# Optimization experiments

Hardware: AMD Instinct MI355X
Metric: run time of the kernel (lower is better)

The kernel has to match this reference:

```python
import math
import jax, jax.numpy as jnp
import numpy as np

D_MODEL = 1024
N_HEADS = 16
HEAD_DIM = 64          # block_size
NUM_RULES = 64
RANK = 8               # proj_rank = round(sqrt(head_dim)); also router_rank
SHARED_RANK = 32       # round(sqrt(d_model))
NUM_BLOCKS = 16        # min(in,out)//block_size = 1024//64; total_block_dim == d_model
B, S = 4, 1024
ROPE_BASE = 10000.0


def setup_inputs() -> dict:
    key = jax.random.key(0)
    ks = iter(jax.random.split(key, 32))
    def nrm(shape, s=0.02):
        return jax.random.normal(next(ks), shape, dtype=jnp.float32) * s
    inp = {
        "x": jax.random.normal(next(ks), (B, S, D_MODEL), dtype=jnp.float32),
        "target_rule_ids": jax.random.randint(next(ks), (B, S), 0, NUM_RULES),
    }
    for p in ("q", "k", "v", "o"):
        inp[p + "_si"] = nrm((D_MODEL, SHARED_RANK))
        inp[p + "_so"] = nrm((SHARED_RANK, D_MODEL))
        inp[p + "_ri"] = nrm((NUM_RULES, HEAD_DIM, RANK))
        inp[p + "_ro"] = nrm((NUM_RULES, RANK, HEAD_DIM))
        inp[p + "_lg"] = nrm((NUM_RULES, NUM_BLOCKS), 1.0 / math.sqrt(NUM_BLOCKS))
    inp["router_q"] = nrm((NUM_RULES, RANK))
    inp["router_k"] = nrm((NUM_RULES, RANK))
    return inp


def _rule_proj(x, rules, si, so, ri, ro, lg):
    """RuleAwareProjection.forward_rules_batched, de-permuted.

    The torch code argsorts tokens by rule, zero-pads per-rule buckets, runs
    bmm per rule and scatters back; mathematically that equals a per-token
    gather of the rule's low-rank adapter, which is what we compute here.
    x: [N, D_MODEL], rules: [N] int.
    """
    base = (x @ si) @ so                                  # shared low-rank path
    xb = x.reshape(-1, NUM_BLOCKS, HEAD_DIM)              # [N, nb, bs]
    h = jnp.einsum('nbs,nsr->nbr', xb, ri[rules])         # [N, nb, rank]
    a = jnp.einsum('nbr,nrt->nbt', h, ro[rules])          # [N, nb, bs]
    # temperature = 1/sqrt(num_blocks) => logits / temperature = logits*sqrt(nb)
    sel = jax.nn.softmax(lg[rules] * math.sqrt(NUM_BLOCKS), axis=-1)
    return base + (a * sel[:, :, None]).reshape(-1, D_MODEL)


def _rope(q, k):
    # q, k: [B, H, S, D]; interleaved-pair rotation, start_pos = 0.
    S_, D = q.shape[2], q.shape[3]
    pos = jnp.arange(S_, dtype=jnp.float32)[:, None]
    div = jnp.exp(jnp.arange(0, D, 2, dtype=jnp.float32) * (-math.log(ROPE_BASE) / D))
    f = pos * div                                         # [S, D/2]
    sin, cos = jnp.sin(f), jnp.cos(f)
    def rot(t):
        t1, t2 = t[..., 0::2], t[..., 1::2]
        return jnp.stack([t1 * cos - t2 * sin, t2 * cos + t1 * sin], axis=-1).reshape(t.shape)
    return rot(q), rot(k)


def reference(x, target_rule_ids,
              q_si, q_so, q_ri, q_ro, q_lg,
              k_si, k_so, k_ri, k_ro, k_lg,
              v_si, v_so, v_ri, v_ro, v_lg,
              o_si, o_so, o_ri, o_ro, o_lg,
              router_q, router_k):
    B_, S_, C = x.shape
    flat_x = x.reshape(-1, C)
    rules = target_rule_ids.reshape(-1)

    q = _rule_proj(flat_x, rules, q_si, q_so, q_ri, q_ro, q_lg)
    k = _rule_proj(flat_x, rules, k_si, k_so, k_ri, k_ro, k_lg)
    v = _rule_proj(flat_x, rules, v_si, v_so, v_ri, v_ro, v_lg)
    q = q.reshape(B_, S_, N_HEADS, HEAD_DIM).transpose(0, 2, 1, 3)
    k = k.reshape(B_, S_, N_HEADS, HEAD_DIM).transpose(0, 2, 1, 3)
    v = v.reshape(B_, S_, N_HEADS, HEAD_DIM).transpose(0, 2, 1, 3)
    q, k = _rope(q, k)

    # rule-routing sparse mask: cosine affinity between token rule embeddings
    rq = router_q[target_rule_ids]                        # [B, S, rank]
    rk = router_k[target_rule_ids]
    rqn = rq / jnp.maximum(jnp.linalg.norm(rq, axis=-1, keepdims=True), 1e-12)
    rkn = rk / jnp.maximum(jnp.linalg.norm(rk, axis=-1, keepdims=True), 1e-12)
    tau = 1.0 / math.log(max(math.e, RANK))
    aff = jnp.einsum('bqr,bkr->bqk', rqn, rkn) / tau       # [B, S, S]
    causal = jnp.tril(jnp.ones((S_, S_), dtype=bool))
    masked = jnp.where(causal[None], aff, -jnp.inf)
    top_k = max(2, int(math.sqrt(S_)))
    if S_ > top_k:
        thr = jax.lax.top_k(masked, top_k)[0][..., -1:]
        rule_mask = (masked >= thr) & causal[None]
    else:
        rule_mask = jnp.broadcast_to(causal[None], masked.shape)

    scores = jnp.einsum('bhqd,bhkd->bhqk', q, k) / math.sqrt(HEAD_DIM)
    scores = jnp.where(rule_mask[:, None], scores, -jnp.inf)
    attn = jax.nn.softmax(scores, axis=-1)
    out = jnp.einsum('bhqk,bhkd->bhqd', attn, v)
    out = out.transpose(0, 2, 1, 3).reshape(-1, C)
    out = _rule_proj(out, rules, o_si, o_so, o_ri, o_ro, o_lg)
    return out.reshape(B_, S_, C)
```

## Files before the change

kernel.cpp:

```cpp
#include <hip/hip_runtime.h>
#include <hip/hip_bf16.h>

#define D_MODEL 1024
#define N_HEADS 16
#define HEAD_DIM 64
#define NUM_RULES 64
#define RANK 8
#define SHARED_RANK 32
#define NUM_BLOCKS_ 16
#define BB 4
#define SS 1024
#define NTOK (BB*SS)
#define NGRP (NTOK/8)
#define NGRP4 (NTOK/4)

typedef __attribute__((ext_vector_type(8))) short bf16x8;
typedef __attribute__((ext_vector_type(4))) float f32x4;

__device__ __forceinline__ float bf2f(unsigned short u) {
  unsigned int i = ((unsigned int)u) << 16;
  float f;
  __builtin_memcpy(&f, &i, 4);
  return f;
}
__device__ __forceinline__ unsigned short f2bf(float f) {
  __hip_bfloat16 h = __float2bfloat16(f);
  unsigned short u;
  __builtin_memcpy(&u, &h, 2);
  return u;
}
__device__ __forceinline__ float u2f(unsigned int i) {
  float f;
  __builtin_memcpy(&f, &i, 4);
  return f;
}
template<bool BF>
__device__ __forceinline__ float ldw(const void* p, size_t i) {
  if (BF) return bf2f(((const unsigned short*)p)[i]);
  else    return ((const float*)p)[i];
}

__global__ void detect_kernel(const unsigned short* __restrict__ x, int* __restrict__ flag) {
  const int lane = threadIdx.x;
  int good = 0;
  for (int i = 0; i < 4; i++) {
    unsigned short u = x[lane*4 + i];
    int e = (u >> 7) & 0xFF;
    good += (e == 0 || (e >= 100 && e <= 145)) ? 1 : 0;
  }
  for (int off = 32; off; off >>= 1) good += __shfl_xor(good, off);
  if (lane == 0) flag[0] = (good >= 224) ? 1 : 0;
}

template<bool BF>
__device__ __forceinline__ void precompute_body(
    const void* rq, const void* rk,
    const void* qlg, const void* klg, const void* vlg, const void* olg,
    float* __restrict__ M, float* __restrict__ sel)
{
  __shared__ float rqn[64][8], rkn[64][8];
  const int tid = threadIdx.x;
  if (tid < 64) {
    float v[8]; float s = 0.f;
    for (int i = 0; i < 8; i++) { v[i] = ldw<BF>(rq, tid*8+i); s += v[i]*v[i]; }
    float inv = 1.0f / fmaxf(sqrtf(s), 1e-12f);
    for (int i = 0; i < 8; i++) rqn[tid][i] = v[i]*inv;
  } else if (tid < 128) {
    int r = tid - 64;
    float v[8]; float s = 0.f;
    for (int i = 0; i < 8; i++) { v[i] = ldw<BF>(rk, r*8+i); s += v[i]*v[i]; }
    float inv = 1.0f / fmaxf(sqrtf(s), 1e-12f);
    for (int i = 0; i < 8; i++) rkn[r][i] = v[i]*inv;
  }
  __syncthreads();
  const float LN8 = 2.0794415416798357f;
  for (int idx = tid; idx < 64*64; idx += 256) {
    int i = idx >> 6, j = idx & 63;
    float d = 0.f;
    for (int t = 0; t < 8; t++) d += rqn[i][t]*rkn[j][t];
    M[idx] = d * LN8;
  }
  const void* lgs[4] = {qlg, klg, vlg, olg};
  {
    int r = tid & 63;
    const void* lg = lgs[tid >> 6];
    float e[NUM_BLOCKS_]; float mx = -1e30f;
    for (int b = 0; b < NUM_BLOCKS_; b++) {
      e[b] = ldw<BF>(lg, r*NUM_BLOCKS_ + b) * 4.0f;
      mx = fmaxf(mx, e[b]);
    }
    float s = 0.f;
    for (int b = 0; b < NUM_BLOCKS_; b++) { e[b] = expf(e[b]-mx); s += e[b]; }
    float inv = 1.0f/s;
    for (int b = 0; b < NUM_BLOCKS_; b++) sel[tid*NUM_BLOCKS_+b] = e[b]*inv;
  }
}

__global__ void precompute_kernel(
    const void* rq, const void* rk,
    const void* qlg, const void* klg, const void* vlg, const void* olg,
    float* M, float* sel, const int* __restrict__ flag)
{
  if (*flag) precompute_body<true >(rq, rk, qlg, klg, vlg, olg, M, sel);
  else       precompute_body<false>(rq, rk, qlg, klg, vlg, olg, M, sel);
}

__global__ __launch_bounds__(128) void prep_wb_kernel(
    const float* __restrict__ qsi, const float* __restrict__ ksi,
    const float* __restrict__ vsi, const float* __restrict__ osi,
    unsigned short* __restrict__ wh, unsigned short* __restrict__ wl,
    const int* __restrict__ flag)
{
  if (*flag) return;
  const int kt = blockIdx.x, p = blockIdx.y;
  const int tid = threadIdx.x, nt = tid >> 6, lane = tid & 63;
  const float* si = (p==0)?qsi:((p==1)?ksi:((p==2)?vsi:osi));
  const int col = nt*16 + (lane & 15);
  const int k0 = kt*32 + (lane >> 4)*8;
  size_t base = ((((size_t)p*32 + kt)*2 + nt)*64 + lane)*8;
  unsigned short h8[8], l8[8];
  #pragma unroll
  for (int j = 0; j < 8; j++) {
    float f = si[(size_t)(k0 + j)*SHARED_RANK + col];
    unsigned short hu = f2bf(f);
    h8[j] = hu;
    l8[j] = f2bf(f - bf2f(hu));
  }
  #pragma unroll
  for (int j = 0; j < 8; j++) { wh[base + j] = h8[j]; wl[base + j] = l8[j]; }
}

template<int NPROJ>
__device__ __forceinline__ void tt_mfma_body(
    const float* __restrict__ xin,
    const unsigned short* __restrict__ wh, const unsigned short* __restrict__ wl,
    int p0, float* __restrict__ ttg)
{
  const int NT = NPROJ*2;
  const int tile = blockIdx.x;
  const int tid = threadIdx.x, lane = tid & 63, w = tid >> 6;
  const int kq = lane >> 4;
  __shared__ float red[4][64][25];

  f32x4 acc[NT];
  #pragma unroll
  for (int i = 0; i < NT; i++) acc[i] = (f32x4){0.f,0.f,0.f,0.f};

  const float* xrow = xin + (size_t)(tile*16 + (lane & 15))*D_MODEL + kq*8;
  #pragma unroll 2
  for (int s = 0; s < 8; s++) {
    const int kt = w*8 + s;
    float4 a0 = *(const float4*)(xrow + kt*32);
    float4 a1 = *(const float4*)(xrow + kt*32 + 4);
    float av[8] = {a0.x,a0.y,a0.z,a0.w,a1.x,a1.y,a1.z,a1.w};
    bf16x8 ah, al;
    #pragma unroll
    for (int j = 0; j < 8; j++) {
      unsigned short hu = f2bf(av[j]);
      ah[j] = (short)hu;
      al[j] = (short)f2bf(av[j] - bf2f(hu));
    }
    #pragma unroll
    for (int p = 0; p < NPROJ; p++) {
      #pragma unroll
      for (int nt = 0; nt < 2; nt++) {
        size_t bidx = ((((size_t)(p0+p)*32 + kt)*2 + nt)*64 + lane)*8;
        bf16x8 bh = *(const bf16x8*)(wh + bidx);
        bf16x8 bl = *(const bf16x8*)(wl + bidx);
        f32x4 c = acc[p*2+nt];
        c = __builtin_amdgcn_mfma_f32_16x16x32_bf16(ah, bh, c, 0, 0, 0);
        c = __builtin_amdgcn_mfma_f32_16x16x32_bf16(al, bh, c, 0, 0, 0);
        c = __builtin_amdgcn_mfma_f32_16x16x32_bf16(ah, bl, c, 0, 0, 0);
        acc[p*2+nt] = c;
      }
    }
  }
  #pragma unroll
  for (int i = 0; i < NT; i++) {
    red[w][lane][i*4+0] = acc[i][0]; red[w][lane][i*4+1] = acc[i][1];
    red[w][lane][i*4+2] = acc[i][2]; red[w][lane][i*4+3] = acc[i][3];
  }
  __syncthreads();
  if (w == 0) {
    const int tok0 = tile*16 + (lane >> 4)*4;
    #pragma unroll
    for (int i = 0; i < NT; i++) {
      const int ys = i >> 1, jj = (i & 1)*16 + (lane & 15);
      #pragma unroll
      for (int r = 0; r < 4; r++) {
        float sum = red[0][lane][i*4+r] + red[1][lane][i*4+r]
                  + red[2][lane][i*4+r] + red[3][lane][i*4+r];
        ttg[((size_t)ys*NTOK + tok0 + r)*32 + jj] = sum;
      }
    }
  }
}

__global__ __launch_bounds__(256) void A_tt_mfma3(
    const float* __restrict__ xin,
    const unsigned short* __restrict__ wh, const unsigned short* __restrict__ wl,
    float* __restrict__ ttg, const int* __restrict__ flag)
{
  if (*flag) return;
  tt_mfma_body<3>(xin, wh, wl, 0, ttg);
}

__global__ __launch_bounds__(256) void A_tt_mfma1(
    const float* __restrict__ xin,
    const unsigned short* __restrict__ wh, const unsigned short* __restrict__ wl,
    float* __restrict__ ttg, const int* __restrict__ flag)
{
  if (*flag) return;
  tt_mfma_body<1>(xin, wh, wl, 3, ttg);
}

template<int NP>
__device__ __forceinline__ void hh_body(
    const float* __restrict__ xin, const int* __restrict__ rules,
    const float* __restrict__ ri0, const float* __restrict__ ri1,
    const float* __restrict__ ri2, float* __restrict__ hhg)
{
  const int g = blockIdx.x, n0 = g*8, tid = threadIdx.x;
  const int t = tid >> 5, blk = (tid >> 1) & 15, r0 = (tid & 1)*4;
  const int n = n0 + t;
  const int rule = rules[n];
  const float* xb = xin + (size_t)n*D_MODEL + blk*64;
  const float* wb[3];
  wb[0] = ri0 + (size_t)rule*512 + r0;
  if (NP > 1) {
    wb[1] = ri1 + (size_t)rule*512 + r0;
    wb[2] = ri2 + (size_t)rule*512 + r0;
  }
  float a[NP][4];
  #pragma unroll
  for (int p = 0; p < NP; p++) { a[p][0]=0.f; a[p][1]=0.f; a[p][2]=0.f; a[p][3]=0.f; }
  #pragma unroll 4
  for (int k4 = 0; k4 < 16; k4++) {
    float4 xv = *(const float4*)(xb + k4*4);
    #pragma unroll
    for (int q = 0; q < 4; q++) {
      const int k = k4*4 + q;
      float xq = (q==0)?xv.x:((q==1)?xv.y:((q==2)?xv.z:xv.w));
      #pragma unroll
      for (int p = 0; p < NP; p++) {
        float4 wv = *(const float4*)(wb[p] + (size_t)k*8);
        a[p][0] += xq*wv.x; a[p][1] += xq*wv.y; a[p][2] += xq*wv.z; a[p][3] += xq*wv.w;
      }
    }
  }
  #pragma unroll
  for (int p = 0; p < NP; p++) {
    float4 hv; hv.x=a[p][0]; hv.y=a[p][1]; hv.z=a[p][2]; hv.w=a[p][3];
    *(float4*)&hhg[((size_t)p*NTOK + n)*128 + blk*8 + r0] = hv;
  }
}

__global__ __launch_bounds__(256) void A_hh3_f32(
    const float* __restrict__ xin, const int* __restrict__ rules,
    const float* __restrict__ qri, const float* __restrict__ kri,
    const float* __restrict__ vri, float* __restrict__ hhg,
    const int* __restrict__ flag)
{
  if (*flag) return;
  hh_body<3>(xin, rules, qri, kri, vri, hhg);
}

__global__ __launch_bounds__(256) void A_hh1_f32(
    const float* __restrict__ xin, const int* __restrict__ rules,
    const float* __restrict__ ori, float* __restrict__ hhg,
    const int* __restrict__ flag)
{
  if (*flag) return;
  hh_body<1>(xin, rules, ori, ori, ori, hhg);
}

template<bool IN_BF, bool W_BF>
__device__ __forceinline__ void stageA_body(
    const void* __restrict__ xin, const int* __restrict__ rules,
    const void* __restrict__ si, const void* __restrict__ ri,
    float* __restrict__ ttg, float* __restrict__ hhg, int yslot)
{
  const int g = blockIdx.x, n0 = g*8, tid = threadIdx.x;
  __shared__ float xs[8][D_MODEL];
  __shared__ float tpart[8][32][9];
  __shared__ int rl[8];

  #pragma unroll
  for (int t = 0; t < 8; t++) {
    float4 f;
    if (IN_BF) {
      ushort4 u = ((const ushort4*)((const unsigned short*)xin + (size_t)(n0+t)*D_MODEL))[tid];
      f.x = bf2f(u.x); f.y = bf2f(u.y); f.z = bf2f(u.z); f.w = bf2f(u.w);
    } else {
      f = ((const float4*)xin)[(size_t)(n0+t)*(D_MODEL/4) + tid];
    }
    *(float4*)&xs[t][tid*4] = f;
  }
  if (tid < 8) rl[tid] = rules[n0 + tid];
  __syncthreads();

  {
    const int c = tid >> 5, j = tid & 31;
    float p[8];
    #pragma unroll
    for (int t = 0; t < 8; t++) p[t] = 0.f;
    #pragma unroll 4
    for (int d4 = 0; d4 < 32; d4++) {
      const int d = c*128 + d4*4;
      float w0 = ldw<W_BF>(si, (size_t)(d+0)*SHARED_RANK + j);
      float w1 = ldw<W_BF>(si, (size_t)(d+1)*SHARED_RANK + j);
      float w2 = ldw<W_BF>(si, (size_t)(d+2)*SHARED_RANK + j);
      float w3 = ldw<W_BF>(si, (size_t)(d+3)*SHARED_RANK + j);
      #pragma unroll
      for (int t = 0; t < 8; t++) {
        float4 xv = *(const float4*)&xs[t][d];
        p[t] += xv.x*w0 + xv.y*w1 + xv.z*w2 + xv.w*w3;
      }
    }
    #pragma unroll
    for (int t = 0; t < 8; t++) tpart[c][j][t] = p[t];
  }
  __syncthreads();

  {
    const int t = tid >> 5, j = tid & 31;
    float s = 0.f;
    #pragma unroll
    for (int c = 0; c < 8; c++) s += tpart[c][j][t];
    ttg[((size_t)yslot*NTOK + n0 + t)*32 + j] = s;
  }
  {
    const int t = tid >> 5, blk = (tid >> 1) & 15, r0 = (tid & 1)*4;
    const int rule = rl[t];
    float a0=0.f, a1=0.f, a2=0.f, a3=0.f;
    #pragma unroll 4
    for (int k4 = 0; k4 < 16; k4++) {
      const int kk = ((k4 + blk) & 15) * 4;
      float4 xv = *(const float4*)&xs[t][blk*64 + kk];
      #pragma unroll
      for (int q = 0; q < 4; q++) {
        const int k = kk + q;
        float w0,w1,w2,w3;
        if (W_BF) {
          ushort4 u = *(const ushort4*)((const unsigned short*)ri + (size_t)rule*512 + (size_t)k*8 + r0);
          w0=bf2f(u.x); w1=bf2f(u.y); w2=bf2f(u.z); w3=bf2f(u.w);
        } else {
          float4 u = *(const float4*)((const float*)ri + (size_t)rule*512 + (size_t)k*8 + r0);
          w0=u.x; w1=u.y; w2=u.z; w3=u.w;
        }
        float xq = (q==0)?xv.x:((q==1)?xv.y:((q==2)?xv.z:xv.w));
        a0 += xq*w0; a1 += xq*w1; a2 += xq*w2; a3 += xq*w3;
      }
    }
    float4 hv; hv.x=a0; hv.y=a1; hv.z=a2; hv.w=a3;
    *(float4*)&hhg[((size_t)yslot*NTOK + n0 + t)*128 + blk*8 + r0] = hv;
  }
}

__global__ __launch_bounds__(256) void A_qkv_bf16(
    const void* x, const int* rules,
    const void* qsi, const void* qri, const void* ksi, const void* kri,
    const void* vsi, const void* vri,
    float* ttg, float* hhg, const int* __restrict__ flag)
{
  if (!*flag) return;
  const int y = blockIdx.y;
  const void* si = (y==0)?qsi:((y==1)?ksi:vsi);
  const void* ri = (y==0)?qri:((y==1)?kri:vri);
  stageA_body<true,true>(x, rules, si, ri, ttg, hhg, y);
}

__global__ __launch_bounds__(256) void A_o_bf16(
    const void* ain, const int* rules, const void* osi, const void* ori,
    float* ttg, float* hhg, const int* __restrict__ flag)
{
  if (!*flag) return;
  stageA_body<false,true>(ain, rules, osi, ori, ttg, hhg, 0);
}

template<bool W_BF>
__device__ __forceinline__ void stageB_body(
    const float* __restrict__ ttg, const float* __restrict__ hhg,
    const int* __restrict__ rules,
    const void* __restrict__ so, const void* __restrict__ ro,
    const float* __restrict__ sel, void* __restrict__ out,
    int yslot, int do_rope, int out_bf)
{
  const int blk4 = blockIdx.x;
  const int n0 = blk4*4, tid = threadIdx.x;
  __shared__ float tt_lds[32][5];
  __shared__ float hh_lds[4][132];
  __shared__ int rl[4];

  if (tid < 128) {
    const int j = tid >> 2, t4 = tid & 3;
    tt_lds[j][t4] = ttg[((size_t)yslot*NTOK + n0 + t4)*32 + j];
  } else if (tid < 256 && (tid - 128) < 128) {
    const int i = tid - 128;
    const int t4 = i >> 5, c = (i*4) & 127;
    float4 hv = *(const float4*)&hhg[((size_t)yslot*NTOK + n0 + t4)*128 + c];
    *(float4*)&hh_lds[t4][c] = hv;
  }
  if (tid < 4) rl[tid] = rules[n0 + tid];
  __syncthreads();

  const int ch0 = tid*4;
  float a0[4], a1[4], a2[4], a3[4];
  #pragma unroll
  for (int t = 0; t < 4; t++) { a0[t]=0.f; a1[t]=0.f; a2[t]=0.f; a3[t]=0.f; }

  #pragma unroll 4
  for (int j = 0; j < 32; j++) {
    float w0, w1, w2, w3;
    if (W_BF) {
      ushort4 u = *(const ushort4*)((const unsigned short*)so + (size_t)j*D_MODEL + ch0);
      w0=bf2f(u.x); w1=bf2f(u.y); w2=bf2f(u.z); w3=bf2f(u.w);
    } else {
      float4 u = *(const float4*)((const float*)so + (size_t)j*D_MODEL + ch0);
      w0=u.x; w1=u.y; w2=u.z; w3=u.w;
    }
    #pragma unroll
    for (int t = 0; t < 4; t++) {
      float tv = tt_lds[j][t];
      a0[t] += tv*w0; a1[t] += tv*w1; a2[t] += tv*w2; a3[t] += tv*w3;
    }
  }

  const int blk = ch0 >> 6, tc = ch0 & 63;
  float inv0 = 0.f, inv1 = 0.f;
  if (do_rope) {
    inv0 = expf(-(float)tc     * (9.210340371976184f/64.0f));
    inv1 = expf(-(float)(tc+2) * (9.210340371976184f/64.0f));
  }
  #pragma unroll 2
  for (int t = 0; t < 4; t++) {
    const int rule = rl[t];
    float b0=0.f, b1=0.f, b2=0.f, b3=0.f;
    #pragma unroll
    for (int r = 0; r < 8; r++) {
      float w0,w1,w2,w3;
      if (W_BF) {
        ushort4 u = *(const ushort4*)((const unsigned short*)ro + (size_t)rule*512 + r*64 + tc);
        w0=bf2f(u.x); w1=bf2f(u.y); w2=bf2f(u.z); w3=bf2f(u.w);
      } else {
        float4 u = *(const float4*)((const float*)ro + (size_t)rule*512 + r*64 + tc);
        w0=u.x; w1=u.y; w2=u.z; w3=u.w;
      }
      float hv = hh_lds[t][blk*8 + r];
      b0 += hv*w0; b1 += hv*w1; b2 += hv*w2; b3 += hv*w3;
    }
    float sb = sel[rule*NUM_BLOCKS_ + blk];
    float e0 = a0[t] + b0*sb, o0 = a1[t] + b1*sb;
    float e1 = a2[t] + b2*sb, o1 = a3[t] + b3*sb;
    const int n = n0 + t;
    if (do_rope) {
      float spos = (float)(n & (SS-1));
      float sn0, cs0, sn1, cs1;
      sincosf(spos*inv0, &sn0, &cs0);
      sincosf(spos*inv1, &sn1, &cs1);
      float u0 = e0*cs0 - o0*sn0; o0 = o0*cs0 + e0*sn0; e0 = u0;
      float u1 = e1*cs1 - o1*sn1; o1 = o1*cs1 + e1*sn1; e1 = u1;
    }
    if (out_bf) {
      ushort4 uv; uv.x=f2bf(e0); uv.y=f2bf(o0); uv.z=f2bf(e1); uv.w=f2bf(o1);
      *(ushort4*)((unsigned short*)out + (size_t)n*D_MODEL + ch0) = uv;
    } else {
      float4 fv; fv.x=e0; fv.y=o0; fv.z=e1; fv.w=o1;
      *(float4*)((float*)out + (size_t)n*D_MODEL + ch0) = fv;
    }
  }
}

__global__ __launch_bounds__(256) void B_qkv(
    const float* ttg, const float* hhg, const int* rules,
    const void* qso, const void* qro, const void* kso, const void* kro,
    const void* vso, const void* vro,
    const float* sel, float* qb, unsigned short* kb, unsigned short* vb,
    const int* __restrict__ flag)
{
  const int y = blockIdx.y;
  const void* so = (y==0)?qso:((y==1)?kso:vso);
  const void* ro = (y==0)?qro:((y==1)?kro:vro);
  void* out = (y==0)?(void*)qb:((y==1)?(void*)kb:(void*)vb);
  if (*flag)
    stageB_body<true >(ttg, hhg, rules, so, ro, sel + y*1024, out, y, (y<2)?1:0, (y>=1)?1:0);
  else
    stageB_body<false>(ttg, hhg, rules, so, ro, sel + y*1024, out, y, (y<2)?1:0, (y>=1)?1:0);
}

__global__ __launch_bounds__(256) void B_o(
    const float* ttg, const float* hhg, const int* rules,
    const void* oso, const void* oro, const float* sel, void* out,
    const int* __restrict__ flag)
{
  if (*flag) stageB_body<true >(ttg, hhg, rules, oso, oro, sel, out, 0, 0, 1);
  else       stageB_body<false>(ttg, hhg, rules, oso, oro, sel, out, 0, 0, 0);
}

__global__ __launch_bounds__(64) void mask_kernel(
    const int* __restrict__ rules, const float* __restrict__ M,
    unsigned long long* __restrict__ am, unsigned int* __restrict__ rp)
{
  const int bid = blockIdx.x;
  const int b = bid >> 10, qi = bid & 1023;
  const int lane = threadIdx.x;
  __shared__ int rrow[SS];
  __shared__ float val[64];
  __shared__ int cnth[64];
  for (int i = lane; i < SS/4; i += 64)
    ((int4*)rrow)[i] = ((const int4*)(rules + b*SS))[i];
  cnth[lane] = 0;
  __syncthreads();
  if (qi < 16 && lane < 16) {
    unsigned v = 0;
    #pragma unroll
    for (int nt = 0; nt < 4; nt++)
      v |= ((unsigned)rrow[qi*64 + nt*16 + lane] & 0xffu) << (8*nt);
    rp[b*256 + qi*16 + lane] = v;
  }
  for (int k = lane; k <= qi; k += 64) atomicAdd(&cnth[rrow[k]], 1);
  const int qrule = rrow[qi];
  const float myv = M[qrule*64 + lane];
  val[lane] = myv;
  __syncthreads();
  const int c = cnth[lane];
  int A = 0;
  for (int r = 0; r < 64; r++) {
    int cr = __shfl(c, r);
    A += (val[r] > myv) ? cr : 0;
  }
  unsigned long long allowed = __ballot(A < 32);
  if (lane == 0) am[bid] = allowed;
}

__global__ __launch_bounds__(256) void vtrans_kernel(
    const unsigned short* __restrict__ vb, unsigned short* __restrict__ vt)
{
  const int st = blockIdx.x, h = blockIdx.y, b = blockIdx.z;
  __shared__ unsigned short t[64][72];
  const int tid = threadIdx.x;
  #pragma unroll
  for (int it = 0; it < 2; it++) {
    int i = tid + it*256;
    int r = i >> 3, c8 = (i & 7)*8;
    uint4 v = *(const uint4*)(vb + ((size_t)(b*SS + st*64 + r)*D_MODEL + h*HEAD_DIM + c8));
    t[c8+0][r] = (unsigned short)(v.x & 0xffffu);
    t[c8+1][r] = (unsigned short)(v.x >> 16);
    t[c8+2][r] = (unsigned short)(v.y & 0xffffu);
    t[c8+3][r] = (unsigned short)(v.y >> 16);
    t[c8+4][r] = (unsigned short)(v.z & 0xffffu);
    t[c8+5][r] = (unsigned short)(v.z >> 16);
    t[c8+6][r] = (unsigned short)(v.w & 0xffffu);
    t[c8+7][r] = (unsigned short)(v.w >> 16);
  }
  __syncthreads();
  #pragma unroll
  for (int it = 0; it < 2; it++) {
    int i = tid + it*256;
    int d = i >> 3, c8 = i & 7;
    uint4 o = *(const uint4*)&t[d][c8*8];
    *(uint4*)(vt + ((size_t)(b*N_HEADS + h)*HEAD_DIM + d)*SS + st*64 + c8*8) = o;
  }
}

__global__ __launch_bounds__(256, 4) void attn_mfma_kernel(
    const float* __restrict__ qb,
    const unsigned short* __restrict__ kb,
    const unsigned short* __restrict__ vtb,
    const unsigned int* __restrict__ rp,
    const unsigned long long* __restrict__ am,
    float* outb)
{
  const int x = blockIdx.x, b = blockIdx.y, h = blockIdx.z;
  const int qt = (x < 8) ? x : (23 - x);
  const int tid = threadIdx.x, lane = tid & 63, w = tid >> 6;
  __shared__ unsigned short Ks[64*64];
  __shared__ unsigned short Vs[64*64];
  __shared__ unsigned short Pl[4][16*64];

  const unsigned short* kbase = kb + (size_t)b*SS*D_MODEL + h*HEAD_DIM;
  const unsigned short* vbase = vtb + (size_t)(b*N_HEADS + h)*HEAD_DIM*SS;
  const unsigned int* rpb = rp + b*256;

  const int srow = tid >> 3;
  const int spos = tid & 7;
  const int kc0 = (srow*8      + (spos ^ (srow        & 7)))*8;
  const int kc1 = ((srow+32)*8 + (spos ^ ((srow+32)   & 7)))*8;
  unsigned short* pw = &Pl[w][0];

  const int qa = qt*64 + w*16 + (lane & 15);
  bf16x8 qfrag[2];
  {
    const float* qrow = qb + (size_t)(b*SS + qa)*D_MODEL + h*HEAD_DIM + (lane>>4)*8;
    #pragma unroll
    for (int kc = 0; kc < 2; kc++) {
      float4 f0 = *(const float4*)(qrow + kc*32);
      float4 f1 = *(const float4*)(qrow + kc*32 + 4);
      bf16x8 qv;
      qv[0] = (short)f2bf(f0.x*0.125f); qv[1] = (short)f2bf(f0.y*0.125f);
      qv[2] = (short)f2bf(f0.z*0.125f); qv[3] = (short)f2bf(f0.w*0.125f);
      qv[4] = (short)f2bf(f1.x*0.125f); qv[5] = (short)f2bf(f1.y*0.125f);
      qv[6] = (short)f2bf(f1.z*0.125f); qv[7] = (short)f2bf(f1.w*0.125f);
      qfrag[kc] = qv;
    }
  }
  int qg[4]; unsigned aqlo[4], aqhi[4];
  #pragma unroll
  for (int r = 0; r < 4; r++) {
    qg[r] = qt*64 + w*16 + (lane>>4)*4 + r;
    uint2 mm = *(const uint2*)(am + (size_t)b*SS + qg[r]);
    aqlo[r] = mm.x; aqhi[r] = mm.y;
  }
  f32x4 Oacc[4];
  #pragma unroll
  for (int nt = 0; nt < 4; nt++) Oacc[nt] = (f32x4){0.f,0.f,0.f,0.f};
  float mrun[4], lrun[4];
  #pragma unroll
  for (int r = 0; r < 4; r++) { mrun[r] = -1e30f; lrun[r] = 0.f; }

  {
    uint4 k0 = *(const uint4*)(kbase + (size_t)srow*D_MODEL + spos*8);
    uint4 k1 = *(const uint4*)(kbase + (size_t)(srow+32)*D_MODEL + spos*8);
    uint4 v0 = *(const uint4*)(vbase + (size_t)srow*SS + spos*8);
    uint4 v1 = *(const uint4*)(vbase + (size_t)(srow+32)*SS + spos*8);
    *(uint4*)&Ks[kc0] = k0; *(uint4*)&Ks[kc1] = k1;
    *(uint4*)&Vs[kc0] = v0; *(uint4*)&Vs[kc1] = v1;
  }
  __syncthreads();

  for (int kt = 0; kt <= qt; kt++) {
    const unsigned ru = rpb[kt*16 + (lane & 15)];
    uint4 nk0, nk1, nv0, nv1;
    if (kt < qt) {
      const size_t koff = (size_t)(kt + 1)*64;
      nk0 = *(const uint4*)(kbase + (koff + srow)*D_MODEL + spos*8);
      nk1 = *(const uint4*)(kbase + (koff + srow + 32)*D_MODEL + spos*8);
      nv0 = *(const uint4*)(vbase + (size_t)srow*SS + koff + spos*8);
      nv1 = *(const uint4*)(vbase + (size_t)(srow+32)*SS + koff + spos*8);
    }

    f32x4 Sacc[4];
    __builtin_amdgcn_s_setprio(1);
    #pragma unroll
    for (int nt = 0; nt < 4; nt++) {
      const int key = nt*16 + (lane & 15);
      f32x4 c = (f32x4){0.f,0.f,0.f,0.f};
      #pragma unroll
      for (int kc = 0; kc < 2; kc++) {
        int off = (key*128 + kc*64 + (lane>>4)*16) ^ ((key & 7) << 4);
        bf16x8 kf = *(const bf16x8*)((const char*)Ks + off);
        c = __builtin_amdgcn_mfma_f32_16x16x32_bf16(qfrag[kc], kf, c, 0, 0, 0);
      }
      Sacc[nt] = c;
    }
    __builtin_amdgcn_s_setprio(0);

    float sv[4][4];
    #pragma unroll
    for (int nt = 0; nt < 4; nt++) {
      const int k = kt*64 + nt*16 + (lane & 15);
      const unsigned rr = (ru >> (nt*8)) & 0xffu;
      const unsigned sh = rr & 31u;
      const bool hi = rr >= 32;
      #pragma unroll
      for (int r = 0; r < 4; r++) {
        unsigned bits = hi ? aqhi[r] : aqlo[r];
        bool ok = (((bits >> sh) & 1u) != 0u) && (k <= qg[r]);
        sv[nt][r] = ok ? Sacc[nt][r] : -3e38f;
      }
    }

    float tm[4];
    #pragma unroll
    for (int r = 0; r < 4; r++)
      tm[r] = fmaxf(fmaxf(sv[0][r], sv[1][r]), fmaxf(sv[2][r], sv[3][r]));
    #pragma unroll
    for (int off = 1; off < 16; off <<= 1) {
      #pragma unroll
      for (int r = 0; r < 4; r++) tm[r] = fmaxf(tm[r], __shfl_xor(tm[r], off));
    }
    float alpha[4];
    #pragma unroll
    for (int r = 0; r < 4; r++) {
      float nm = fmaxf(mrun[r], tm[r]);
      alpha[r] = __expf(mrun[r] - nm);
      mrun[r] = nm;
    }
    float ps[4] = {0.f, 0.f, 0.f, 0.f};
    #pragma unroll
    for (int nt = 0; nt < 4; nt++) {
      #pragma unroll
      for (int r = 0; r < 4; r++) {
        float p = __expf(sv[nt][r] - mrun[r]);
        ps[r] += p;
        const int q = (lane>>4)*4 + r;
        int off = (q*128 + (nt*16 + (lane & 15))*2) ^ ((q & 7) << 4);
        *(unsigned short*)((char*)pw + off) = f2bf(p);
      }
    }
    #pragma unroll
    for (int off = 1; off < 16; off <<= 1) {
      #pragma unroll
      for (int r = 0; r < 4; r++) ps[r] += __shfl_xor(ps[r], off);
    }
    #pragma unroll
    for (int r = 0; r < 4; r++) lrun[r] = lrun[r]*alpha[r] + ps[r];
    #pragma unroll
    for (int nt = 0; nt < 4; nt++) {
      Oacc[nt][0] *= alpha[0]; Oacc[nt][1] *= alpha[1];
      Oacc[nt][2] *= alpha[2]; Oacc[nt][3] *= alpha[3];
    }

    __builtin_amdgcn_s_setprio(1);
    #pragma unroll
    for (int kc = 0; kc < 2; kc++) {
      const int qrow = lane & 15;
      int aoff = (qrow*128 + kc*64 + (lane>>4)*16) ^ ((qrow & 7) << 4);
      bf16x8 pa = *(const bf16x8*)((const char*)pw + aoff);
      #pragma unroll
      for (int nt = 0; nt < 4; nt++) {
        const int d = nt*16 + (lane & 15);
        int boff = (d*128 + kc*64 + (lane>>4)*16) ^ ((d & 7) << 4);
        bf16x8 vf = *(const bf16x8*)((const char*)Vs + boff);
        Oacc[nt] = __builtin_amdgcn_mfma_f32_16x16x32_bf16(pa, vf, Oacc[nt], 0, 0, 0);
      }
    }
    __builtin_amdgcn_s_setprio(0);
    __syncthreads();
    if (kt < qt) {
      *(uint4*)&Ks[kc0] = nk0; *(uint4*)&Ks[kc1] = nk1;
      *(uint4*)&Vs[kc0] = nv0; *(uint4*)&Vs[kc1] = nv1;
      __syncthreads();
    }
  }

  float invl[4];
  #pragma unroll
  for (int r = 0; r < 4; r++) invl[r] = 1.0f / lrun[r];
  #pragma unroll
  for (int nt = 0; nt < 4; nt++) {
    #pragma unroll
    for (int r = 0; r < 4; r++) {
      outb[(size_t)(b*SS + qg[r])*D_MODEL + h*HEAD_DIM + nt*16 + (lane & 15)]
          = Oacc[nt][r]*invl[r];
    }
  }
}

extern "C" void kernel_launch(void* const* d_in, const int* in_sizes, int n_in,
                              void* d_out, int out_size, void* d_ws, size_t ws_size,
                              hipStream_t stream) {
  (void)in_sizes; (void)n_in; (void)out_size; (void)ws_size;
  const void* x    = d_in[0];
  const int* rules = (const int*)d_in[1];
  const void* q_si = d_in[2];  const void* q_so = d_in[3];
  const void* q_ri = d_in[4];  const void* q_ro = d_in[5];  const void* q_lg = d_in[6];
  const void* k_si = d_in[7];  const void* k_so = d_in[8];
  const void* k_ri = d_in[9];  const void* k_ro = d_in[10]; const void* k_lg = d_in[11];
  const void* v_si = d_in[12]; const void* v_so = d_in[13];
  const void* v_ri = d_in[14]; const void* v_ro = d_in[15]; const void* v_lg = d_in[16];
  const void* o_si = d_in[17]; const void* o_so = d_in[18];
  const void* o_ri = d_in[19]; const void* o_ro = d_in[20]; const void* o_lg = d_in[21];
  const void* rq   = d_in[22]; const void* rk   = d_in[23];

  char* ws = (char*)d_ws;
  const size_t MB = 1024*1024;
  float*          qb    = (float*)(ws);
  unsigned short* kb    = (unsigned short*)(ws + 16*MB);
  unsigned short* vb    = (unsigned short*)(ws + 24*MB);
  unsigned short* vtb   = (unsigned short*)(ws + 32*MB);
  float*          ttg   = (float*)(ws + 40*MB);
  float*          hhg   = (float*)(ws + 42*MB);
  unsigned long long* amask = (unsigned long long*)(ws + 48*MB);
  float*          Mt    = (float*)(ws + 49*MB + 16*1024);
  float*          selt  = (float*)(ws + 49*MB + 32*1024);
  int*            flag  = (int*)  (ws + 49*MB + 48*1024);
  unsigned int*   rp    = (unsigned int*)(ws + 49*MB + 52*1024);
  unsigned short* wpkh  = (unsigned short*)(ws + 49*MB + 64*1024);
  unsigned short* wpkl  = (unsigned short*)(ws + 49*MB + 64*1024 + 256*1024);

  detect_kernel<<<1, 64, 0, stream>>>((const unsigned short*)x, flag);
  precompute_kernel<<<1, 256, 0, stream>>>(rq, rk, q_lg, k_lg, v_lg, o_lg, Mt, selt, flag);
  mask_kernel<<<NTOK, 64, 0, stream>>>(rules, Mt, amask, rp);
  prep_wb_kernel<<<dim3(32, 4), 128, 0, stream>>>(
      (const float*)q_si, (const float*)k_si, (const float*)v_si, (const float*)o_si,
      wpkh, wpkl, flag);

  A_qkv_bf16<<<dim3(NGRP, 3), 256, 0, stream>>>(x, rules, q_si, q_ri, k_si, k_ri, v_si, v_ri, ttg, hhg, flag);
  A_tt_mfma3<<<256, 256, 0, stream>>>((const float*)x, wpkh, wpkl, ttg, flag);
  A_hh3_f32<<<NGRP, 256, 0, stream>>>((const float*)x, rules,
      (const float*)q_ri, (const float*)k_ri, (const float*)v_ri, hhg, flag);

  B_qkv<<<dim3(NGRP4, 3), 256, 0, stream>>>(ttg, hhg, rules, q_so, q_ro, k_so, k_ro, v_so, v_ro,
                                            selt, qb, kb, vb, flag);

  vtrans_kernel<<<dim3(16, 16, 4), 256, 0, stream>>>(vb, vtb);
  attn_mfma_kernel<<<dim3(16, BB, N_HEADS), 256, 0, stream>>>(qb, kb, vtb, rp, amask, qb);

  A_o_bf16<<<dim3(NGRP, 1), 256, 0, stream>>>(qb, rules, o_si, o_ri, ttg, hhg, flag);
  A_tt_mfma1<<<256, 256, 0, stream>>>(qb, wpkh, wpkl, ttg, flag);
  A_hh1_f32<<<NGRP, 256, 0, stream>>>(qb, rules, (const float*)o_ri, hhg, flag);
  B_o<<<NGRP4, 256, 0, stream>>>(ttg, hhg, rules, o_so, o_ro, selt + 3*1024, d_out, flag);
}
```

Baseline: 284.6 us.

## Split long causal attention query tiles across two blocks with combine pass

Query tiles 9..15 now have their key range split into two halves, each handled by a separate block that writes unnormalized fp16 partial outputs plus running max and sum to a workspace buffer. A new combine kernel merges the two partials with log-sum-exp rescaling into the final output. The grid grows from 16 to 23 tiles per (batch, head), and launch bounds raise occupancy to 6 blocks per CU. The goal is to balance per-block causal work and shorten the tail. The cost is an extra launch, an extra workspace round trip, and fp16 rounding of the partial accumulators.

```diff
diff --git a/kernel.cpp b/kernel.cpp
--- a/kernel.cpp
+++ b/kernel.cpp
@@ -1,5 +1,6 @@
 #include <hip/hip_runtime.h>
 #include <hip/hip_bf16.h>
+#include <hip/hip_fp16.h>
 
 #define D_MODEL 1024
 #define N_HEADS 16
@@ -29,10 +30,16 @@
   __builtin_memcpy(&u, &h, 2);
   return u;
 }
-__device__ __forceinline__ float u2f(unsigned int i) {
-  float f;
-  __builtin_memcpy(&f, &i, 4);
-  return f;
+__device__ __forceinline__ unsigned short f2h(float f) {
+  __half h = __float2half(f);
+  unsigned short u;
+  __builtin_memcpy(&u, &h, 2);
+  return u;
+}
+__device__ __forceinline__ float h2f(unsigned short u) {
+  __half h;
+  __builtin_memcpy(&h, &u, 2);
+  return __half2float(h);
 }
 template<bool BF>
 __device__ __forceinline__ float ldw(const void* p, size_t i) {
@@ -563,16 +570,26 @@
   }
 }
 
-__global__ __launch_bounds__(256, 4) void attn_mfma_kernel(
+__global__ __launch_bounds__(256, 6) void attn_mfma_kernel(
     const float* __restrict__ qb,
     const unsigned short* __restrict__ kb,
     const unsigned short* __restrict__ vtb,
     const unsigned int* __restrict__ rp,
     const unsigned long long* __restrict__ am,
+    unsigned short* __restrict__ Obuf,
+    float* __restrict__ mlbuf,
     float* outb)
 {
   const int x = blockIdx.x, b = blockIdx.y, h = blockIdx.z;
-  const int qt = (x < 8) ? x : (23 - x);
+  int qt, k0t, k1t, pidx;
+  bool partial;
+  if (x < 9) { qt = x; k0t = 0; k1t = qt; partial = false; pidx = 0; }
+  else {
+    const int j = x - 9, qti = j >> 1, s = j & 1;
+    qt = 9 + qti; partial = true;
+    pidx = ((b*N_HEADS + h)*7 + qti)*2 + s;
+    if (s == 0) { k0t = 0; k1t = 7; } else { k0t = 8; k1t = qt; }
+  }
   const int tid = threadIdx.x, lane = tid & 63, w = tid >> 6;
   __shared__ unsigned short Ks[64*64];
   __shared__ unsigned short Vs[64*64];
@@ -619,19 +636,20 @@
   for (int r = 0; r < 4; r++) { mrun[r] = -1e30f; lrun[r] = 0.f; }
 
   {
-    uint4 k0 = *(const uint4*)(kbase + (size_t)srow*D_MODEL + spos*8);
-    uint4 k1 = *(const uint4*)(kbase + (size_t)(srow+32)*D_MODEL + spos*8);
-    uint4 v0 = *(const uint4*)(vbase + (size_t)srow*SS + spos*8);
-    uint4 v1 = *(const uint4*)(vbase + (size_t)(srow+32)*SS + spos*8);
+    const size_t koff0 = (size_t)k0t*64;
+    uint4 k0 = *(const uint4*)(kbase + (koff0 + srow)*D_MODEL + spos*8);
+    uint4 k1 = *(const uint4*)(kbase + (koff0 + srow + 32)*D_MODEL + spos*8);
+    uint4 v0 = *(const uint4*)(vbase + (size_t)srow*SS + koff0 + spos*8);
+    uint4 v1 = *(const uint4*)(vbase + (size_t)(srow+32)*SS + koff0 + spos*8);
     *(uint4*)&Ks[kc0] = k0; *(uint4*)&Ks[kc1] = k1;
     *(uint4*)&Vs[kc0] = v0; *(uint4*)&Vs[kc1] = v1;
   }
   __syncthreads();
 
-  for (int kt = 0; kt <= qt; kt++) {
+  for (int kt = k0t; kt <= k1t; kt++) {
     const unsigned ru = rpb[kt*16 + (lane & 15)];
     uint4 nk0, nk1, nv0, nv1;
-    if (kt < qt) {
+    if (kt < k1t) {
       const size_t koff = (size_t)(kt + 1)*64;
       nk0 = *(const uint4*)(kbase + (koff + srow)*D_MODEL + spos*8);
       nk1 = *(const uint4*)(kbase + (koff + srow + 32)*D_MODEL + spos*8);
@@ -727,23 +745,74 @@
     }
     __builtin_amdgcn_s_setprio(0);
     __syncthreads();
-    if (kt < qt) {
+    if (kt < k1t) {
       *(uint4*)&Ks[kc0] = nk0; *(uint4*)&Ks[kc1] = nk1;
       *(uint4*)&Vs[kc0] = nv0; *(uint4*)&Vs[kc1] = nv1;
       __syncthreads();
     }
   }
 
-  float invl[4];
-  #pragma unroll
-  for (int r = 0; r < 4; r++) invl[r] = 1.0f / lrun[r];
-  #pragma unroll
-  for (int nt = 0; nt < 4; nt++) {
-    #pragma unroll
-    for (int r = 0; r < 4; r++) {
-      outb[(size_t)(b*SS + qg[r])*D_MODEL + h*HEAD_DIM + nt*16 + (lane & 15)]
-          = Oacc[nt][r]*invl[r];
-    }
+  if (!partial) {
+    float invl[4];
+    #pragma unroll
+    for (int r = 0; r < 4; r++) invl[r] = 1.0f / lrun[r];
+    #pragma unroll
+    for (int nt = 0; nt < 4; nt++) {
+      #pragma unroll
+      for (int r = 0; r < 4; r++) {
+        outb[(size_t)(b*SS + qg[r])*D_MODEL + h*HEAD_DIM + nt*16 + (lane & 15)]
+            = Oacc[nt][r]*invl[r];
+      }
+    }
+  } else {
+    unsigned short* ob = Obuf + (size_t)pidx*4096;
+    #pragma unroll
+    for (int nt = 0; nt < 4; nt++) {
+      #pragma unroll
+      for (int r = 0; r < 4; r++) {
+        const int row = w*16 + (lane>>4)*4 + r;
+        ob[row*64 + nt*16 + (lane & 15)] = f2h(Oacc[nt][r]);
+      }
+    }
+    if ((lane & 15) == 0) {
+      float* ml = mlbuf + (size_t)pidx*128;
+      #pragma unroll
+      for (int r = 0; r < 4; r++) {
+        const int row = w*16 + (lane>>4)*4 + r;
+        ml[row]      = mrun[r];
+        ml[64 + row] = lrun[r];
+      }
+    }
+  }
+}
+
+__global__ __launch_bounds__(256) void attn_combine(
+    const unsigned short* __restrict__ Obuf, const float* __restrict__ mlbuf,
+    float* __restrict__ outb)
+{
+  const int qti = blockIdx.x, b = blockIdx.y, h = blockIdx.z;
+  const int qt = 9 + qti;
+  const int p0 = ((b*N_HEADS + h)*7 + qti)*2;
+  const int tid = threadIdx.x;
+  const int row = tid >> 2, c0 = (tid & 3)*16;
+  const float* ml0 = mlbuf + (size_t)p0*128;
+  const float* ml1 = mlbuf + (size_t)(p0+1)*128;
+  const float m0 = ml0[row], l0 = ml0[64+row];
+  const float m1 = ml1[row], l1 = ml1[64+row];
+  const float M = fmaxf(m0, m1);
+  const float w0 = __expf(m0 - M), w1 = __expf(m1 - M);
+  const float inv = 1.0f / (w0*l0 + w1*l1);
+  const unsigned short* o0 = Obuf + (size_t)p0*4096 + row*64 + c0;
+  const unsigned short* o1 = Obuf + (size_t)(p0+1)*4096 + row*64 + c0;
+  float* dst = outb + (size_t)(b*SS + qt*64 + row)*D_MODEL + h*HEAD_DIM + c0;
+  #pragma unroll
+  for (int j = 0; j < 16; j += 4) {
+    float4 fv;
+    fv.x = (w0*h2f(o0[j+0]) + w1*h2f(o1[j+0]))*inv;
+    fv.y = (w0*h2f(o0[j+1]) + w1*h2f(o1[j+1]))*inv;
+    fv.z = (w0*h2f(o0[j+2]) + w1*h2f(o1[j+2]))*inv;
+    fv.w = (w0*h2f(o0[j+3]) + w1*h2f(o1[j+3]))*inv;
+    *(float4*)(dst + j) = fv;
   }
 }
 
@@ -771,6 +840,8 @@
   unsigned short* vtb   = (unsigned short*)(ws + 32*MB);
   float*          ttg   = (float*)(ws + 40*MB);
   float*          hhg   = (float*)(ws + 42*MB);
+  unsigned short* Obuf  = (unsigned short*)(ws + 40*MB);
+  float*          mlbuf = (float*)(ws + 47*MB);
   unsigned long long* amask = (unsigned long long*)(ws + 48*MB);
   float*          Mt    = (float*)(ws + 49*MB + 16*1024);
   float*          selt  = (float*)(ws + 49*MB + 32*1024);
@@ -795,7 +866,9 @@
                                             selt, qb, kb, vb, flag);
 
   vtrans_kernel<<<dim3(16, 16, 4), 256, 0, stream>>>(vb, vtb);
-  attn_mfma_kernel<<<dim3(16, BB, N_HEADS), 256, 0, stream>>>(qb, kb, vtb, rp, amask, qb);
+  attn_mfma_kernel<<<dim3(23, BB, N_HEADS), 256, 0, stream>>>(qb, kb, vtb, rp, amask,
+                                                              Obuf, mlbuf, qb);
+  attn_combine<<<dim3(7, BB, N_HEADS), 256, 0, stream>>>(Obuf, mlbuf, qb);
 
   A_o_bf16<<<dim3(NGRP, 1), 256, 0, stream>>>(qb, rules, o_si, o_ri, ttg, hhg, flag);
   A_tt_mfma1<<<256, 256, 0, stream>>>(qb, wpkh, wpkl, ttg, flag);
```

New measurement: 381.4 us. +34.0%, slower.
